# Optimization experiments

Measured on AMD Instinct MI355X. Metric: run time of the kernel, lower is better.

## Reference

```python
import jax, jax.numpy as jnp
import numpy as np

B, L, D, DFF = 4, 4096, 1024, 4096
EPS = 1e-6

def _rmsnorm(x, w):
    return x * jax.lax.rsqrt(jnp.mean(x * x, axis=-1, keepdims=True) + EPS) * w

def setup_inputs() -> dict:
    key = jax.random.key(0)
    ks = jax.random.split(key, 16)
    s = 1.0 / np.sqrt(D)
    sf = 1.0 / np.sqrt(DFF)
    return {
        "x": jax.random.normal(ks[0], (B, L, D), jnp.float32),
        # QuasiLSTM gate linears, stored [in, out]; y = x @ W + b
        "w_forget": jax.random.normal(ks[1], (D, D), jnp.float32) * s,
        "b_forget": jnp.zeros((D,), jnp.float32),
        "w_input": jax.random.normal(ks[2], (D, D), jnp.float32) * s,
        "b_input": jnp.zeros((D,), jnp.float32),
        "w_igate": jax.random.normal(ks[3], (D, D), jnp.float32) * s,
        "b_igate": jnp.zeros((D,), jnp.float32),
        "w_ogate": jax.random.normal(ks[4], (D, D), jnp.float32) * s,
        "b_ogate": jnp.zeros((D,), jnp.float32),
        "h0": jax.random.normal(ks[5], (D,), jnp.float32),  # last_hidden_init
        "norm1_w": jnp.ones((D,), jnp.float32),
        "norm2_w": jnp.ones((D,), jnp.float32),
        # FFN SwiGLU
        "w_fc": jax.random.normal(ks[6], (D, DFF), jnp.float32) * s,
        "b_fc": jnp.zeros((DFF,), jnp.float32),
        "w_fc_act": jax.random.normal(ks[7], (D, DFF), jnp.float32) * s,
        "b_fc_act": jnp.zeros((DFF,), jnp.float32),
        "w_out": jax.random.normal(ks[8], (DFF, D), jnp.float32) * sf,
        "b_out": jnp.zeros((D,), jnp.float32),
    }

def reference(x, w_forget, b_forget, w_input, b_input, w_igate, b_igate,
              w_ogate, b_ogate, h0, norm1_w, norm2_w,
              w_fc, b_fc, w_fc_act, b_fc_act, w_out, b_out):
    # --- QuasiLSTM branch (pre-norm residual) ---
    x_res = x
    xn = _rmsnorm(x, norm1_w)                                   # [B,L,D]
    forget = jax.nn.sigmoid(xn @ w_forget + b_forget)           # a_t
    inp = jnp.tanh(xn @ w_input + b_input) * jax.nn.sigmoid(xn @ w_igate + b_igate)  # b_t
    # Linear recurrence h_t = a_t * h_{t-1} + b_t, h_0 = 0 (inner chunk),
    # computed as an associative scan over the length axis.
    def comb(left, right):
        a_l, b_l = left
        a_r, b_r = right
        return (a_l * a_r, b_l * a_r + b_r)
    _, h_inner = jax.lax.associative_scan(comb, (forget, inp), axis=1)
    # cross-chunk contribution from last_hidden_init
    h = h_inner + h0[None, None, :] * jnp.cumprod(forget, axis=1)
    y = jnp.tanh(h) * jax.nn.sigmoid(xn @ w_ogate + b_ogate)
    x1 = y + x_res  # dropout p=0 -> identity
    # --- FFN SwiGLU branch ---
    xn2 = _rmsnorm(x1, norm2_w)
    hff = (xn2 @ w_fc + b_fc) * jax.nn.silu(xn2 @ w_fc_act + b_fc_act)
    out = hff @ w_out + b_out
    return out + x1
```

## Files before the change

### kernel.cpp

```cpp
#include <hip/hip_runtime.h>
#include <math.h>
#include <stdint.h>

static constexpr int Bb  = 4;
static constexpr int Ll  = 4096;
static constexpr int Dd  = 1024;
static constexpr int DFF = 4096;
static constexpr int Mm  = Bb * Ll;
static constexpr int CH  = 64;
static constexpr int CS  = Ll / CH;
static constexpr float EPS = 1e-6f;

typedef __attribute__((ext_vector_type(8))) short short8;
typedef __attribute__((ext_vector_type(4))) float floatx4;
typedef __attribute__((ext_vector_type(4))) unsigned short us4;

__device__ __forceinline__ float sigmoidf_(float v) { return 1.0f / (1.0f + __expf(-v)); }
__device__ __forceinline__ float fast_tanh(float x) {
    return 2.0f / (1.0f + __expf(-2.0f * x)) - 1.0f;
}
__device__ __forceinline__ ushort f2bf(float f) {
    union { float f; uint32_t u; } v; v.f = f;
    return (ushort)((v.u + 0x7FFFu + ((v.u >> 16) & 1u)) >> 16);
}
__device__ __forceinline__ float bf2f(ushort h) {
    union { uint32_t u; float f; } v; v.u = (uint32_t)h << 16; return v.f;
}

__device__ __forceinline__ void gload16(const ushort* g, ushort* l) {
    __builtin_amdgcn_global_load_lds(
        (const __attribute__((address_space(1))) uint32_t*)g,
        (__attribute__((address_space(3))) uint32_t*)l, 16, 0, 0);
}

static constexpr int HT_US  = 256 * 32;
static constexpr int BUF_US = 4 * HT_US;

__device__ __forceinline__ void gemm_core_8ph(
    const ushort* __restrict__ A, const ushort* __restrict__ B1,
    const ushort* __restrict__ B2, int m0, int n0b1, int n0b2, int K,
    ushort* lds, floatx4 (&acc1)[8][2], floatx4 (&acc2)[8][2])
{
    const int tid = threadIdx.x;
    const int mm = tid >> 2, ss = tid & 3;
    const int kb = ss ^ ((mm >> 1) & 3);
    const ushort* pA0 = A  + (size_t)(m0 + mm) * K + kb * 8;
    const ushort* pA1 = pA0 + (size_t)128 * K;
    const ushort* pB0 = B1 + (size_t)(n0b1 + mm) * K + kb * 8;
    const ushort* pB1 = B2 + (size_t)(n0b2 + mm) * K + kb * 8;

    const int wave = tid >> 6, lane = tid & 63;
    const int wr = wave >> 2, wc = wave & 3;
    const int fr = lane & 15, q = lane >> 4;
    const int slot8 = (q ^ ((fr >> 1) & 3)) << 3;
    const int aoff  = (wr * 128 + fr) * 32 + slot8;
    const int boff  = 2 * HT_US + (wc * 32 + fr) * 32 + slot8;

    const int NT = K >> 6;

#define STG_A(bsel, kk, tt) do { \
        ushort* d_ = lds + (bsel) * BUF_US + (kk) * HT_US; \
        int o_ = (tt) * 64 + (kk) * 32; \
        gload16(pA0 + o_, d_ + tid * 8); \
        gload16(pA1 + o_, d_ + (tid + 512) * 8); } while (0)
#define STG_B(bsel, kk, tt) do { \
        ushort* d_ = lds + (bsel) * BUF_US + (2 + (kk)) * HT_US; \
        int o_ = (tt) * 64 + (kk) * 32; \
        gload16(pB0 + o_, d_ + tid * 8); \
        gload16(pB1 + o_, d_ + (tid + 512) * 8); } while (0)
#define MFMA_HALF(mh) do { \
        __builtin_amdgcn_s_setprio(1); \
        _Pragma("unroll") \
        for (int i_ = 0; i_ < 4; ++i_) { \
            acc1[(mh)*4+i_][0] = __builtin_amdgcn_mfma_f32_16x16x32_bf16(a[i_], b[0], acc1[(mh)*4+i_][0], 0, 0, 0); \
            acc2[(mh)*4+i_][0] = __builtin_amdgcn_mfma_f32_16x16x32_bf16(a[i_], c[0], acc2[(mh)*4+i_][0], 0, 0, 0); \
            acc1[(mh)*4+i_][1] = __builtin_amdgcn_mfma_f32_16x16x32_bf16(a[i_], b[1], acc1[(mh)*4+i_][1], 0, 0, 0); \
            acc2[(mh)*4+i_][1] = __builtin_amdgcn_mfma_f32_16x16x32_bf16(a[i_], c[1], acc2[(mh)*4+i_][1], 0, 0, 0); \
        } \
        __builtin_amdgcn_s_setprio(0); } while (0)

    STG_A(0, 0, 0); STG_B(0, 0, 0); STG_A(0, 1, 0); STG_B(0, 1, 0);
    asm volatile("s_waitcnt vmcnt(4)" ::: "memory");
    __builtin_amdgcn_s_barrier();

    for (int t = 0; t < NT; ++t) {
        const int buf = t & 1, nbuf = buf ^ 1;
        const bool pf = (t + 1 < NT);
        const ushort* Ab = lds + buf * BUF_US;
        short8 a[4], b[2], c[2];

        #pragma unroll
        for (int i = 0; i < 4; ++i) a[i] = *(const short8*)&Ab[aoff + i * 512];
        #pragma unroll
        for (int n = 0; n < 2; ++n) {
            b[n] = *(const short8*)&Ab[boff + n * 512];
            c[n] = *(const short8*)&Ab[boff + 4096 + n * 512];
        }
        if (pf) STG_A(nbuf, 0, t + 1);
        __builtin_amdgcn_s_barrier();
        MFMA_HALF(0);
        __builtin_amdgcn_s_barrier();

        #pragma unroll
        for (int i = 0; i < 4; ++i) a[i] = *(const short8*)&Ab[aoff + (i + 4) * 512];
        if (pf) STG_B(nbuf, 0, t + 1);
        __builtin_amdgcn_s_barrier();
        MFMA_HALF(1);
        if (pf) asm volatile("s_waitcnt vmcnt(4)" ::: "memory");
        else    asm volatile("s_waitcnt vmcnt(0)" ::: "memory");
        __builtin_amdgcn_s_barrier();

        const ushort* Ab1 = Ab + HT_US;
        #pragma unroll
        for (int i = 0; i < 4; ++i) a[i] = *(const short8*)&Ab1[aoff + i * 512];
        #pragma unroll
        for (int n = 0; n < 2; ++n) {
            b[n] = *(const short8*)&Ab1[boff + n * 512];
            c[n] = *(const short8*)&Ab1[boff + 4096 + n * 512];
        }
        if (pf) STG_A(nbuf, 1, t + 1);
        __builtin_amdgcn_s_barrier();
        MFMA_HALF(0);
        __builtin_amdgcn_s_barrier();

        #pragma unroll
        for (int i = 0; i < 4; ++i) a[i] = *(const short8*)&Ab1[aoff + (i + 4) * 512];
        if (pf) STG_B(nbuf, 1, t + 1);
        __builtin_amdgcn_s_barrier();
        MFMA_HALF(1);
        if (pf) asm volatile("s_waitcnt vmcnt(4)" ::: "memory");
        __builtin_amdgcn_s_barrier();
    }
#undef STG_A
#undef STG_B
#undef MFMA_HALF
}

__global__ __launch_bounds__(512) void mfma_gemm_gates(
    const ushort* __restrict__ A, const ushort* __restrict__ W1t,
    const ushort* __restrict__ W2t,
    const float* __restrict__ b_input, const float* __restrict__ b_forget,
    const float* __restrict__ b_igate, const float* __restrict__ b_ogate,
    ushort* __restrict__ Ga, ushort* __restrict__ Gb, ushort* __restrict__ Gog)
{
    __shared__ __align__(16) ushort lds[2 * BUF_US];
    int xcd = blockIdx.x & 7, i = blockIdx.x >> 3;
    int bx = xcd * 2 + (i & 1), by = i >> 1;
    int m0 = by * 256, n0 = bx * 128;

    floatx4 acc1[8][2] = {};
    floatx4 acc2[8][2] = {};
    gemm_core_8ph(A, W1t, W2t, m0, n0, n0, Dd, lds, acc1, acc2);

    int tid = threadIdx.x, wave = tid >> 6, lane = tid & 63;
    int wr = wave >> 2, wc = wave & 3, fr = lane & 15, q = lane >> 4;
    #pragma unroll
    for (int ni = 0; ni < 2; ++ni) {
        int col = n0 + wc * 32 + ni * 16 + fr;
        if (col < 1024) {
            float b1v = b_input[col], b2v = b_igate[col];
            #pragma unroll
            for (int mi = 0; mi < 8; ++mi)
                #pragma unroll
                for (int r = 0; r < 4; ++r) {
                    int row = m0 + wr * 128 + mi * 16 + q * 4 + r;
                    float z1 = acc1[mi][ni][r] + b1v;
                    float z2 = acc2[mi][ni][r] + b2v;
                    Gb[(size_t)row * Dd + col] = f2bf(fast_tanh(z1) * sigmoidf_(z2));
                }
        } else {
            int c2 = col - 1024;
            float b1v = b_forget[c2], b2v = b_ogate[c2];
            #pragma unroll
            for (int mi = 0; mi < 8; ++mi)
                #pragma unroll
                for (int r = 0; r < 4; ++r) {
                    int row = m0 + wr * 128 + mi * 16 + q * 4 + r;
                    float z1 = acc1[mi][ni][r] + b1v;
                    float z2 = acc2[mi][ni][r] + b2v;
                    Ga[(size_t)row * Dd + c2]  = f2bf(sigmoidf_(z1));
                    Gog[(size_t)row * Dd + c2] = f2bf(sigmoidf_(z2));
                }
        }
    }
}

__global__ __launch_bounds__(512) void mfma_gemm_swiglu(
    const ushort* __restrict__ A, const ushort* __restrict__ W1t,
    const float* __restrict__ b1, const ushort* __restrict__ W2t,
    const float* __restrict__ b2, ushort* __restrict__ C)
{
    __shared__ __align__(16) ushort lds[2 * BUF_US];
    int xcd = blockIdx.x & 7, i = blockIdx.x >> 3;
    int bx = xcd * 4 + (i & 3), by = i >> 2;
    int m0 = by * 256, n0 = bx * 128;

    floatx4 acc1[8][2] = {};
    floatx4 acc2[8][2] = {};
    gemm_core_8ph(A, W1t, W2t, m0, n0, n0, Dd, lds, acc1, acc2);

    int tid = threadIdx.x, wave = tid >> 6, lane = tid & 63;
    int wr = wave >> 2, wc = wave & 3, fr = lane & 15, q = lane >> 4;
    #pragma unroll
    for (int ni = 0; ni < 2; ++ni) {
        int col = n0 + wc * 32 + ni * 16 + fr;
        float b1v = b1[col], b2v = b2[col];
        #pragma unroll
        for (int mi = 0; mi < 8; ++mi)
            #pragma unroll
            for (int r = 0; r < 4; ++r) {
                int row = m0 + wr * 128 + mi * 16 + q * 4 + r;
                float z1 = acc1[mi][ni][r] + b1v;
                float z2 = acc2[mi][ni][r] + b2v;
                C[(size_t)row * DFF + col] = f2bf(z1 * z2 * sigmoidf_(z2));
            }
    }
}

__global__ __launch_bounds__(512) void mfma_gemm_residual(
    const ushort* __restrict__ A, const ushort* __restrict__ Wt,
    const float* __restrict__ bias, float* __restrict__ C)
{
    __shared__ __align__(16) ushort lds[2 * BUF_US];
    int xcd = blockIdx.x & 7, i = blockIdx.x >> 3;
    int s = xcd * 32 + i;
    int bx = s & 3, by = s >> 2;
    int m0 = by * 256, n0 = bx * 256;

    floatx4 acc1[8][2] = {};
    floatx4 acc2[8][2] = {};
    gemm_core_8ph(A, Wt, Wt, m0, n0, n0 + 128, DFF, lds, acc1, acc2);

    int tid = threadIdx.x, wave = tid >> 6, lane = tid & 63;
    int wr = wave >> 2, wc = wave & 3, fr = lane & 15, q = lane >> 4;
    #pragma unroll
    for (int ni = 0; ni < 2; ++ni) {
        int col1 = n0 + wc * 32 + ni * 16 + fr;
        int col2 = col1 + 128;
        float bs1 = bias[col1], bs2 = bias[col2];
        #pragma unroll
        for (int mi = 0; mi < 8; ++mi)
            #pragma unroll
            for (int r = 0; r < 4; ++r) {
                int row = m0 + wr * 128 + mi * 16 + q * 4 + r;
                size_t i1 = (size_t)row * Dd + col1;
                size_t i2 = (size_t)row * Dd + col2;
                C[i1] = acc1[mi][ni][r] + bs1 + C[i1];
                C[i2] = acc2[mi][ni][r] + bs2 + C[i2];
            }
    }
}

__global__ __launch_bounds__(256) void transpose_cast_kernel(
    const float* __restrict__ W, ushort* __restrict__ Wt, int K, int N)
{
    __shared__ float t[32][33];
    int lx = threadIdx.x & 31, ly = threadIdx.x >> 5;
    int n = blockIdx.x * 32 + lx;
    #pragma unroll
    for (int i = 0; i < 4; ++i) {
        int k = blockIdx.y * 32 + ly + i * 8;
        t[ly + i * 8][lx] = W[(size_t)k * N + n];
    }
    __syncthreads();
    int k2 = blockIdx.y * 32 + lx;
    #pragma unroll
    for (int i = 0; i < 4; ++i) {
        int n2 = blockIdx.x * 32 + ly + i * 8;
        Wt[(size_t)n2 * K + k2] = f2bf(t[lx][ly + i * 8]);
    }
}

__global__ __launch_bounds__(256) void transpose_cast_gates(
    const float* __restrict__ w_i, const float* __restrict__ w_f,
    const float* __restrict__ w_g, const float* __restrict__ w_o,
    ushort* __restrict__ W1t, ushort* __restrict__ W2t)
{
    int z = blockIdx.z;
    const float* W = (z == 0) ? w_i : (z == 1) ? w_f : (z == 2) ? w_g : w_o;
    ushort* Wt = (z == 0) ? W1t : (z == 1) ? W1t + (size_t)1024 * Dd
               : (z == 2) ? W2t : W2t + (size_t)1024 * Dd;
    __shared__ float t[32][33];
    int lx = threadIdx.x & 31, ly = threadIdx.x >> 5;
    int n = blockIdx.x * 32 + lx;
    #pragma unroll
    for (int i = 0; i < 4; ++i) {
        int k = blockIdx.y * 32 + ly + i * 8;
        t[ly + i * 8][lx] = W[(size_t)k * Dd + n];
    }
    __syncthreads();
    int k2 = blockIdx.y * 32 + lx;
    #pragma unroll
    for (int i = 0; i < 4; ++i) {
        int n2 = blockIdx.x * 32 + ly + i * 8;
        Wt[(size_t)n2 * Dd + k2] = f2bf(t[lx][ly + i * 8]);
    }
}

__global__ __launch_bounds__(256) void rmsnorm_bf16_kernel(
    const float* __restrict__ x, const float* __restrict__ w,
    ushort* __restrict__ o)
{
    int row = blockIdx.x;
    int tid = threadIdx.x;
    float4 v = ((const float4*)(x + (size_t)row * Dd))[tid];
    float ss = v.x*v.x + v.y*v.y + v.z*v.z + v.w*v.w;
    #pragma unroll
    for (int off = 32; off > 0; off >>= 1) ss += __shfl_down(ss, off, 64);
    __shared__ float red[4];
    if ((tid & 63) == 0) red[tid >> 6] = ss;
    __syncthreads();
    float scale = rsqrtf((red[0] + red[1] + red[2] + red[3]) * (1.0f / Dd) + EPS);
    float4 wv = ((const float4*)w)[tid];
    us4 ov;
    ov.x = f2bf(v.x * scale * wv.x);
    ov.y = f2bf(v.y * scale * wv.y);
    ov.z = f2bf(v.z * scale * wv.z);
    ov.w = f2bf(v.w * scale * wv.w);
    *(us4*)&o[(size_t)row * Dd + tid * 4] = ov;
}

__global__ __launch_bounds__(256) void scan_pass1(
    const ushort* __restrict__ Ga, const ushort* __restrict__ Gb,
    float* __restrict__ P, float* __restrict__ Hend)
{
    int tid = threadIdx.x;
    int c = blockIdx.x, b = blockIdx.y;
    size_t base = ((size_t)b * Ll + (size_t)c * CS) * Dd + tid * 4;
    float p[4] = {1.f, 1.f, 1.f, 1.f};
    float h[4] = {};
    #pragma unroll 4
    for (int t = 0; t < CS; ++t) {
        us4 av = *(const us4*)&Ga[base + (size_t)t * Dd];
        us4 bv = *(const us4*)&Gb[base + (size_t)t * Dd];
        #pragma unroll
        for (int j = 0; j < 4; ++j) {
            float aa = bf2f(av[j]);
            float bb = bf2f(bv[j]);
            p[j] *= aa;
            h[j] = aa * h[j] + bb;
        }
    }
    size_t o = ((size_t)b * CH + c) * Dd + tid * 4;
    *(float4*)&P[o]    = make_float4(p[0], p[1], p[2], p[3]);
    *(float4*)&Hend[o] = make_float4(h[0], h[1], h[2], h[3]);
}

__global__ __launch_bounds__(256) void scan_pass2(
    const float* __restrict__ P, const float* __restrict__ Hend,
    const float* __restrict__ h0, float* __restrict__ Carry)
{
    int idx = blockIdx.x * 256 + threadIdx.x;
    int b = idx / Dd, d = idx % Dd;
    float carry = h0[d];
    for (int c = 0; c < CH; ++c) {
        size_t o = ((size_t)b * CH + c) * Dd + d;
        Carry[o] = carry;
        carry = P[o] * carry + Hend[o];
    }
}

__global__ __launch_bounds__(256) void scan_pass3_norm(
    const ushort* __restrict__ Ga, const ushort* __restrict__ Gb,
    const ushort* __restrict__ Gog, const float* __restrict__ Carry,
    const float* __restrict__ x, const float* __restrict__ norm2w,
    float* __restrict__ x1, ushort* __restrict__ xnb)
{
    int tid = threadIdx.x;
    int c = blockIdx.x, b = blockIdx.y;
    size_t base = ((size_t)b * Ll + (size_t)c * CS) * Dd + tid * 4;
    float4 h4 = *(const float4*)&Carry[((size_t)b * CH + c) * Dd + tid * 4];
    float h[4] = {h4.x, h4.y, h4.z, h4.w};
    float4 w4 = ((const float4*)norm2w)[tid];
    float wv[4] = {w4.x, w4.y, w4.z, w4.w};
    __shared__ float red[4];

    for (int t = 0; t < CS; ++t) {
        size_t i = base + (size_t)t * Dd;
        us4 av = *(const us4*)&Ga[i];
        us4 bv = *(const us4*)&Gb[i];
        us4 gv = *(const us4*)&Gog[i];
        float4 xv = *(const float4*)&x[i];
        float xs[4] = {xv.x, xv.y, xv.z, xv.w};
        float v[4];
        #pragma unroll
        for (int j = 0; j < 4; ++j) {
            float aa = bf2f(av[j]);
            float bb = bf2f(bv[j]);
            h[j] = aa * h[j] + bb;
            v[j] = fast_tanh(h[j]) * bf2f(gv[j]) + xs[j];
        }
        *(float4*)&x1[i] = make_float4(v[0], v[1], v[2], v[3]);
        float ss = v[0]*v[0] + v[1]*v[1] + v[2]*v[2] + v[3]*v[3];
        #pragma unroll
        for (int off = 32; off > 0; off >>= 1) ss += __shfl_down(ss, off, 64);
        if ((tid & 63) == 0) red[tid >> 6] = ss;
        __syncthreads();
        float scale = rsqrtf((red[0] + red[1] + red[2] + red[3]) * (1.0f / Dd) + EPS);
        us4 ov;
        #pragma unroll
        for (int j = 0; j < 4; ++j) ov[j] = f2bf(v[j] * scale * wv[j]);
        *(us4*)&xnb[i] = ov;
        __syncthreads();
    }
}

extern "C" void kernel_launch(void* const* d_in, const int* in_sizes, int n_in,
                              void* d_out, int out_size, void* d_ws, size_t ws_size,
                              hipStream_t stream)
{
    const float* x        = (const float*)d_in[0];
    const float* w_forget = (const float*)d_in[1];
    const float* b_forget = (const float*)d_in[2];
    const float* w_input  = (const float*)d_in[3];
    const float* b_input  = (const float*)d_in[4];
    const float* w_igate  = (const float*)d_in[5];
    const float* b_igate  = (const float*)d_in[6];
    const float* w_ogate  = (const float*)d_in[7];
    const float* b_ogate  = (const float*)d_in[8];
    const float* h0       = (const float*)d_in[9];
    const float* norm1_w  = (const float*)d_in[10];
    const float* norm2_w  = (const float*)d_in[11];
    const float* w_fc     = (const float*)d_in[12];
    const float* b_fc     = (const float*)d_in[13];
    const float* w_fc_act = (const float*)d_in[14];
    const float* b_fc_act = (const float*)d_in[15];
    const float* w_out    = (const float*)d_in[16];
    const float* b_out    = (const float*)d_in[17];
    float* out = (float*)d_out;

    char* ws = (char*)d_ws;
    const size_t MB = 1ull << 20;
    ushort* wtG1  = (ushort*)(ws + 0 * MB);
    ushort* wtG2  = (ushort*)(ws + 4 * MB);
    ushort* wtFC  = (ushort*)(ws + 8 * MB);
    ushort* wtFCA = (ushort*)(ws + 16 * MB);
    ushort* wtOUT = (ushort*)(ws + 24 * MB);
    ushort* xnb   = (ushort*)(ws + 32 * MB);
    ushort* Ga    = (ushort*)(ws + 64 * MB);
    ushort* Gb    = (ushort*)(ws + 96 * MB);
    ushort* Gog   = (ushort*)(ws + 128 * MB);
    ushort* hff   = (ushort*)(ws + 64 * MB);
    float*  P     = (float*)(ws + 192 * MB);
    float*  Hend  = (float*)(ws + 193 * MB);
    float*  Carry = (float*)(ws + 194 * MB);

    transpose_cast_gates<<<dim3(32, 32, 4), 256, 0, stream>>>(
        w_input, w_forget, w_igate, w_ogate, wtG1, wtG2);
    transpose_cast_kernel<<<dim3(DFF/32, Dd/32), 256, 0, stream>>>(w_fc,     wtFC,  Dd, DFF);
    transpose_cast_kernel<<<dim3(DFF/32, Dd/32), 256, 0, stream>>>(w_fc_act, wtFCA, Dd, DFF);
    transpose_cast_kernel<<<dim3(Dd/32, DFF/32), 256, 0, stream>>>(w_out,    wtOUT, DFF, Dd);

    rmsnorm_bf16_kernel<<<Mm, 256, 0, stream>>>(x, norm1_w, xnb);

    mfma_gemm_gates<<<(2048/128) * (Mm/256), 512, 0, stream>>>(
        xnb, wtG1, wtG2, b_input, b_forget, b_igate, b_ogate, Ga, Gb, Gog);

    dim3 sg(CH, Bb);
    scan_pass1<<<sg, 256, 0, stream>>>(Ga, Gb, P, Hend);
    scan_pass2<<<(Bb * Dd) / 256, 256, 0, stream>>>(P, Hend, h0, Carry);
    scan_pass3_norm<<<sg, 256, 0, stream>>>(Ga, Gb, Gog, Carry, x, norm2_w,
                                            out, xnb);

    mfma_gemm_swiglu<<<(DFF/128) * (Mm/256), 512, 0, stream>>>(
        xnb, wtFC, b_fc, wtFCA, b_fc_act, hff);

    mfma_gemm_residual<<<(Dd/256) * (Mm/256), 512, 0, stream>>>(
        hff, wtOUT, b_out, out);
}
```

Before: 852.2 us.

## Collapse eight-phase GEMM main loop into two-phase pipeline with fewer barriers

The shared GEMM core used by all three matmul kernels is restructured. Each K-tile now issues all eight async global-to-LDS loads for the next tile at once and reads all eight A fragments per half. It then runs the full MFMA block per half, and vmcnt waits are tuned so the second half of the prefetch is only awaited in the next iteration. This removes most of the per-tile workgroup barriers and the fine-grained interleaving of loads with MFMA. In exchange it raises register pressure and gives coarser overlap between memory traffic and compute.

```diff
diff --git a/kernel.cpp b/kernel.cpp
--- a/kernel.cpp
+++ b/kernel.cpp
@@ -36,7 +36,7 @@
 static constexpr int HT_US  = 256 * 32;
 static constexpr int BUF_US = 4 * HT_US;
 
-__device__ __forceinline__ void gemm_core_8ph(
+__device__ __forceinline__ void gemm_core_2ph(
     const ushort* __restrict__ A, const ushort* __restrict__ B1,
     const ushort* __restrict__ B2, int m0, int n0b1, int n0b2, int K,
     ushort* lds, floatx4 (&acc1)[8][2], floatx4 (&acc2)[8][2])
@@ -58,82 +58,74 @@
 
     const int NT = K >> 6;
 
-#define STG_A(bsel, kk, tt) do { \
-        ushort* d_ = lds + (bsel) * BUF_US + (kk) * HT_US; \
-        int o_ = (tt) * 64 + (kk) * 32; \
-        gload16(pA0 + o_, d_ + tid * 8); \
-        gload16(pA1 + o_, d_ + (tid + 512) * 8); } while (0)
-#define STG_B(bsel, kk, tt) do { \
-        ushort* d_ = lds + (bsel) * BUF_US + (2 + (kk)) * HT_US; \
-        int o_ = (tt) * 64 + (kk) * 32; \
-        gload16(pB0 + o_, d_ + tid * 8); \
-        gload16(pB1 + o_, d_ + (tid + 512) * 8); } while (0)
-#define MFMA_HALF(mh) do { \
+#define STG_TILE(bsel, tt) do { \
+        ushort* dA0 = lds + (bsel) * BUF_US; \
+        ushort* dA1 = dA0 + HT_US; \
+        ushort* dB0 = dA0 + 2 * HT_US; \
+        ushort* dB1 = dA0 + 3 * HT_US; \
+        int o0 = (tt) * 64, o1 = o0 + 32; \
+        gload16(pA0 + o0, dA0 + tid * 8); gload16(pA1 + o0, dA0 + (tid + 512) * 8); \
+        gload16(pB0 + o0, dB0 + tid * 8); gload16(pB1 + o0, dB0 + (tid + 512) * 8); \
+        gload16(pA0 + o1, dA1 + tid * 8); gload16(pA1 + o1, dA1 + (tid + 512) * 8); \
+        gload16(pB0 + o1, dB1 + tid * 8); gload16(pB1 + o1, dB1 + (tid + 512) * 8); } while (0)
+
+#define READ_FRAGS(base) do { \
+        _Pragma("unroll") \
+        for (int i_ = 0; i_ < 8; ++i_) a[i_] = *(const short8*)&(base)[aoff + i_ * 512]; \
+        _Pragma("unroll") \
+        for (int n_ = 0; n_ < 2; ++n_) { \
+            b[n_] = *(const short8*)&(base)[boff + n_ * 512]; \
+            c[n_] = *(const short8*)&(base)[boff + 4096 + n_ * 512]; \
+        } } while (0)
+
+#define MFMA_FULL() do { \
         __builtin_amdgcn_s_setprio(1); \
         _Pragma("unroll") \
-        for (int i_ = 0; i_ < 4; ++i_) { \
-            acc1[(mh)*4+i_][0] = __builtin_amdgcn_mfma_f32_16x16x32_bf16(a[i_], b[0], acc1[(mh)*4+i_][0], 0, 0, 0); \
-            acc2[(mh)*4+i_][0] = __builtin_amdgcn_mfma_f32_16x16x32_bf16(a[i_], c[0], acc2[(mh)*4+i_][0], 0, 0, 0); \
-            acc1[(mh)*4+i_][1] = __builtin_amdgcn_mfma_f32_16x16x32_bf16(a[i_], b[1], acc1[(mh)*4+i_][1], 0, 0, 0); \
-            acc2[(mh)*4+i_][1] = __builtin_amdgcn_mfma_f32_16x16x32_bf16(a[i_], c[1], acc2[(mh)*4+i_][1], 0, 0, 0); \
+        for (int mi_ = 0; mi_ < 8; ++mi_) { \
+            acc1[mi_][0] = __builtin_amdgcn_mfma_f32_16x16x32_bf16(a[mi_], b[0], acc1[mi_][0], 0, 0, 0); \
+            acc2[mi_][0] = __builtin_amdgcn_mfma_f32_16x16x32_bf16(a[mi_], c[0], acc2[mi_][0], 0, 0, 0); \
+            acc1[mi_][1] = __builtin_amdgcn_mfma_f32_16x16x32_bf16(a[mi_], b[1], acc1[mi_][1], 0, 0, 0); \
+            acc2[mi_][1] = __builtin_amdgcn_mfma_f32_16x16x32_bf16(a[mi_], c[1], acc2[mi_][1], 0, 0, 0); \
         } \
         __builtin_amdgcn_s_setprio(0); } while (0)
 
-    STG_A(0, 0, 0); STG_B(0, 0, 0); STG_A(0, 1, 0); STG_B(0, 1, 0);
+    STG_TILE(0, 0);
     asm volatile("s_waitcnt vmcnt(4)" ::: "memory");
     __builtin_amdgcn_s_barrier();
 
-    for (int t = 0; t < NT; ++t) {
+    int t = 0;
+    for (; t < NT - 1; ++t) {
         const int buf = t & 1, nbuf = buf ^ 1;
-        const bool pf = (t + 1 < NT);
         const ushort* Ab = lds + buf * BUF_US;
-        short8 a[4], b[2], c[2];
-
-        #pragma unroll
-        for (int i = 0; i < 4; ++i) a[i] = *(const short8*)&Ab[aoff + i * 512];
-        #pragma unroll
-        for (int n = 0; n < 2; ++n) {
-            b[n] = *(const short8*)&Ab[boff + n * 512];
-            c[n] = *(const short8*)&Ab[boff + 4096 + n * 512];
-        }
-        if (pf) STG_A(nbuf, 0, t + 1);
+        short8 a[8], b[2], c[2];
+
+        READ_FRAGS(Ab);
+        STG_TILE(nbuf, t + 1);
+        MFMA_FULL();
+        asm volatile("s_waitcnt vmcnt(8)" ::: "memory");
         __builtin_amdgcn_s_barrier();
-        MFMA_HALF(0);
+
+        const ushort* Ab1 = Ab + HT_US;
+        READ_FRAGS(Ab1);
+        MFMA_FULL();
+        asm volatile("s_waitcnt vmcnt(4)" ::: "memory");
         __builtin_amdgcn_s_barrier();
-
-        #pragma unroll
-        for (int i = 0; i < 4; ++i) a[i] = *(const short8*)&Ab[aoff + (i + 4) * 512];
-        if (pf) STG_B(nbuf, 0, t + 1);
+    }
+    {
+        const int buf = t & 1;
+        const ushort* Ab = lds + buf * BUF_US;
+        short8 a[8], b[2], c[2];
+        READ_FRAGS(Ab);
+        MFMA_FULL();
+        asm volatile("s_waitcnt vmcnt(0)" ::: "memory");
         __builtin_amdgcn_s_barrier();
-        MFMA_HALF(1);
-        if (pf) asm volatile("s_waitcnt vmcnt(4)" ::: "memory");
-        else    asm volatile("s_waitcnt vmcnt(0)" ::: "memory");
-        __builtin_amdgcn_s_barrier();
-
         const ushort* Ab1 = Ab + HT_US;
-        #pragma unroll
-        for (int i = 0; i < 4; ++i) a[i] = *(const short8*)&Ab1[aoff + i * 512];
-        #pragma unroll
-        for (int n = 0; n < 2; ++n) {
-            b[n] = *(const short8*)&Ab1[boff + n * 512];
-            c[n] = *(const short8*)&Ab1[boff + 4096 + n * 512];
-        }
-        if (pf) STG_A(nbuf, 1, t + 1);
-        __builtin_amdgcn_s_barrier();
-        MFMA_HALF(0);
-        __builtin_amdgcn_s_barrier();
-
-        #pragma unroll
-        for (int i = 0; i < 4; ++i) a[i] = *(const short8*)&Ab1[aoff + (i + 4) * 512];
-        if (pf) STG_B(nbuf, 1, t + 1);
-        __builtin_amdgcn_s_barrier();
-        MFMA_HALF(1);
-        if (pf) asm volatile("s_waitcnt vmcnt(4)" ::: "memory");
-        __builtin_amdgcn_s_barrier();
-    }
-#undef STG_A
-#undef STG_B
-#undef MFMA_HALF
+        READ_FRAGS(Ab1);
+        MFMA_FULL();
+    }
+#undef STG_TILE
+#undef READ_FRAGS
+#undef MFMA_FULL
 }
 
 __global__ __launch_bounds__(512) void mfma_gemm_gates(
@@ -150,7 +142,7 @@
 
     floatx4 acc1[8][2] = {};
     floatx4 acc2[8][2] = {};
-    gemm_core_8ph(A, W1t, W2t, m0, n0, n0, Dd, lds, acc1, acc2);
+    gemm_core_2ph(A, W1t, W2t, m0, n0, n0, Dd, lds, acc1, acc2);
 
     int tid = threadIdx.x, wave = tid >> 6, lane = tid & 63;
     int wr = wave >> 2, wc = wave & 3, fr = lane & 15, q = lane >> 4;
@@ -197,7 +189,7 @@
 
     floatx4 acc1[8][2] = {};
     floatx4 acc2[8][2] = {};
-    gemm_core_8ph(A, W1t, W2t, m0, n0, n0, Dd, lds, acc1, acc2);
+    gemm_core_2ph(A, W1t, W2t, m0, n0, n0, Dd, lds, acc1, acc2);
 
     int tid = threadIdx.x, wave = tid >> 6, lane = tid & 63;
     int wr = wave >> 2, wc = wave & 3, fr = lane & 15, q = lane >> 4;
@@ -229,7 +221,7 @@
 
     floatx4 acc1[8][2] = {};
     floatx4 acc2[8][2] = {};
-    gemm_core_8ph(A, Wt, Wt, m0, n0, n0 + 128, DFF, lds, acc1, acc2);
+    gemm_core_2ph(A, Wt, Wt, m0, n0, n0 + 128, DFF, lds, acc1, acc2);
 
     int tid = threadIdx.x, wave = tid >> 6, lane = tid & 63;
     int wr = wave >> 2, wc = wave & 3, fr = lane & 15, q = lane >> 4;
```

After: 873.5 us. 2.5% more time.
